# Kernel optimization log

Hardware: AMD Instinct MI355X
Metric: run time of the kernel (lower is better)

Reference implementation:

```python
import jax, jax.numpy as jnp
import numpy as np

N = 50000
E = 800000
IN_DIM = 128
LABEL_DIM = 32
D_MODEL = 128
REL_DIM = 32
NUM_LABELS = 1000
REL_BUCKETS = 1024
N_LAYERS = 2
EPS = 1e-5


def setup_inputs() -> dict:
    key = jax.random.key(0)
    ks = jax.random.split(key, 16)
    s = 0.02
    return {
        "x": jax.random.normal(ks[0], (N, IN_DIM), jnp.float32),
        "label": jax.random.randint(ks[1], (N,), 0, NUM_LABELS),
        "edge_index": jax.random.randint(ks[2], (2, E), 0, N),
        "edge_rel": jax.random.randint(ks[3], (E,), 0, REL_BUCKETS),
        "label_emb": jax.random.normal(ks[4], (NUM_LABELS, LABEL_DIM), jnp.float32) * s,
        "in_proj_w": jax.random.normal(ks[5], (IN_DIM + LABEL_DIM, D_MODEL), jnp.float32) * s,
        "in_proj_b": jnp.zeros((D_MODEL,), jnp.float32),
        "rel_emb": jax.random.normal(ks[6], (N_LAYERS, REL_BUCKETS, REL_DIM), jnp.float32) * s,
        "lin_neigh_w": jax.random.normal(ks[7], (N_LAYERS, D_MODEL, D_MODEL), jnp.float32) * s,
        "lin_self_w": jax.random.normal(ks[8], (N_LAYERS, D_MODEL, D_MODEL), jnp.float32) * s,
        "lin_self_b": jnp.zeros((N_LAYERS, D_MODEL), jnp.float32),
        "lin_rel_w": jax.random.normal(ks[9], (N_LAYERS, REL_DIM, D_MODEL), jnp.float32) * s,
        "ln_g": jnp.ones((N_LAYERS, D_MODEL), jnp.float32),
        "ln_b": jnp.zeros((N_LAYERS, D_MODEL), jnp.float32),
    }


def _layernorm(x, g, b):
    mu = jnp.mean(x, axis=-1, keepdims=True)
    var = jnp.mean(jnp.square(x - mu), axis=-1, keepdims=True)
    return (x - mu) * jax.lax.rsqrt(var + EPS) * g + b


def reference(x, label, edge_index, edge_rel, label_emb, in_proj_w, in_proj_b,
              rel_emb, lin_neigh_w, lin_self_w, lin_self_b, lin_rel_w, ln_g, ln_b):
    n = x.shape[0]
    src, dst = edge_index[0], edge_index[1]
    # input projection
    h = jnp.concatenate([x, label_emb[label]], axis=-1) @ in_proj_w + in_proj_b
    h = jax.nn.relu(h)
    # in-degree for mean aggregation (PyG 'mean' gives 0 for isolated nodes)
    deg = jax.ops.segment_sum(jnp.ones((src.shape[0],), h.dtype), dst, num_segments=n)
    inv_deg = jnp.where(deg > 0, 1.0 / jnp.maximum(deg, 1.0), 0.0)[:, None]
    for l in range(N_LAYERS):
        rel = rel_emb[l][edge_rel]                                   # [E, rel_dim]
        msg = h[src] @ lin_neigh_w[l] + rel @ lin_rel_w[l]           # [E, d]
        agg = jax.ops.segment_sum(msg, dst, num_segments=n) * inv_deg
        out = h @ lin_self_w[l] + lin_self_b[l] + agg
        h = _layernorm(jax.nn.relu(out), ln_g[l], ln_b[l])
    return h
```

## Files before the change

### kernel.cpp

```cpp
#include <hip/hip_runtime.h>
#include <hip/hip_bf16.h>

#define N_NODES 50000
#define N_EDGES 800000
#define D 128
#define LABEL_DIM 32
#define REL_DIM 32
#define REL_BUCKETS 1024
#define NUM_LABELS 1000
#define LN_EPS 1e-5f

#define NB 196
#define CAP 6144
#define EPB 1024

#define PB_IN 80
#define PB_LEMB 125
#define PB_CAT 144
#define PREP_UNITS (PB_IN + PB_LEMB + 2 * PB_CAT)

typedef short bf16x8 __attribute__((ext_vector_type(8)));
typedef float f32x4 __attribute__((ext_vector_type(4)));

__device__ inline unsigned short f2bf(float f) {
    __hip_bfloat16 h = __float2bfloat16(f);
    return *reinterpret_cast<unsigned short*>(&h);
}
__device__ inline float bf2f(unsigned short u) {
    return __uint_as_float((unsigned)u << 16);
}

__global__ __launch_bounds__(256) void prep_all_kernel(
    const float* __restrict__ in_proj_w, const float* __restrict__ label_emb,
    const float* __restrict__ lin_neigh_w, const float* __restrict__ lin_self_w,
    const float* __restrict__ lin_rel_w,
    unsigned short* __restrict__ Btx, unsigned short* __restrict__ leb,
    unsigned short* __restrict__ Btc0, unsigned short* __restrict__ Btc1,
    int* __restrict__ gcur) {
    int bb = blockIdx.x;
    const int t = threadIdx.x;
    if (bb == PREP_UNITS) {
        if (t < NB) gcur[t] = 0;
        return;
    }
    if (bb < PB_IN) {
        int idx = bb * 256 + t;
        int n = idx / 160, k = idx % 160;
        Btx[idx] = f2bf(in_proj_w[k * 128 + n]);
        return;
    }
    bb -= PB_IN;
    if (bb < PB_LEMB) {
        int i = bb * 256 + t;
        if (i < NUM_LABELS * LABEL_DIM) leb[i] = f2bf(label_emb[i]);
        return;
    }
    bb -= PB_LEMB;
    {
        int l = bb >= PB_CAT;
        if (l) bb -= PB_CAT;
        int idx = bb * 256 + t;
        int n = idx / 288, k = idx % 288;
        const float* Ws = lin_self_w + (size_t)l * 128 * 128;
        const float* Wn = lin_neigh_w + (size_t)l * 128 * 128;
        const float* Wr = lin_rel_w + (size_t)l * REL_DIM * 128;
        float v = (k < 128) ? Ws[(size_t)k * 128 + n]
                : (k < 256) ? Wn[(size_t)(k - 128) * 128 + n]
                            : Wr[(size_t)(k - 256) * 128 + n];
        (l ? Btc1 : Btc0)[idx] = f2bf(v);
    }
}

__global__ __launch_bounds__(256) void bin_scatter_kernel(const int* __restrict__ src,
                                                          const int* __restrict__ dst,
                                                          const int* __restrict__ rel,
                                                          int* __restrict__ gcur,
                                                          unsigned* __restrict__ staged_pk,
                                                          unsigned char* __restrict__ staged_dl) {
    __shared__ int hist[NB];
    __shared__ int lcur[NB];
    const int t = threadIdx.x;
    for (int i = t; i < NB; i += 256) hist[i] = 0;
    __syncthreads();
    const int e0 = blockIdx.x * EPB;
    unsigned char bb[4], dl[4];
#pragma unroll
    for (int i = 0; i < 4; ++i) {
        int e = e0 + i * 256 + t;
        if (e < N_EDGES) {
            int d = dst[e];
            bb[i] = (unsigned char)(d >> 8);
            dl[i] = (unsigned char)(d & 255);
            atomicAdd(&hist[d >> 8], 1);
        }
    }
    __syncthreads();
    for (int b = t; b < NB; b += 256) {
        int hc = hist[b];
        lcur[b] = hc ? (b * CAP + atomicAdd(&gcur[b], hc)) : 0;
    }
    __syncthreads();
#pragma unroll
    for (int i = 0; i < 4; ++i) {
        int e = e0 + i * 256 + t;
        if (e < N_EDGES) {
            int pos = atomicAdd(&lcur[bb[i]], 1);
            staged_pk[pos] = (unsigned)src[e] | ((unsigned)rel[e] << 16);
            staged_dl[pos] = dl[i];
        }
    }
}

__global__ __launch_bounds__(256) void place_in_kernel(
    const int* __restrict__ gcur,
    const unsigned* __restrict__ staged_pk, const unsigned char* __restrict__ staged_dl,
    int* __restrict__ off, int* __restrict__ deg, unsigned* __restrict__ csr_pk,
    const float* __restrict__ X, const unsigned short* __restrict__ Btx,
    const unsigned short* __restrict__ leb, const int* __restrict__ label,
    const float* __restrict__ bias, unsigned short* __restrict__ hb) {
    __shared__ __align__(16) char smem[128 * 160 * 2];
    const int t = threadIdx.x;
    const int bid = blockIdx.x;

    if (bid < NB) {
        int* ph = (int*)smem;
        int* pbuf = ph + 256;
        int* pcur = pbuf + 256;
        const int beg = bid * CAP;
        const int end = beg + gcur[bid];
        ph[t] = 0;
        __syncthreads();
        for (int i = beg + t; i < end; i += 256) atomicAdd(&ph[staged_dl[i]], 1);
        __syncthreads();
        int v = ph[t];
        pbuf[t] = v;
        __syncthreads();
        for (int o = 1; o < 256; o <<= 1) {
            int tv = (t >= o) ? pbuf[t - o] : 0;
            __syncthreads();
            pbuf[t] += tv;
            __syncthreads();
        }
        int node_off = beg + pbuf[t] - v;
        int node = bid * 256 + t;
        if (node < N_NODES) {
            off[node] = node_off;
            deg[node] = v;
        }
        pcur[t] = node_off;
        __syncthreads();
        for (int i = beg + t; i < end; i += 256) {
            int pos = atomicAdd(&pcur[staged_dl[i]], 1);
            csr_pk[pos] = staged_pk[i];
        }
        return;
    }

    unsigned short* sB = (unsigned short*)smem;
    const int mb = bid - NB;
#pragma unroll
    for (int i = 0; i < 10; ++i) {
        int c = t + i * 256;
        int col = c / 20, kch = c % 20;
        int dstc = col * 20 + (kch < 16 ? (kch ^ (col & 7)) : kch);
        *(bf16x8*)&sB[dstc * 8] = *(const bf16x8*)&Btx[c * 8];
    }
    __syncthreads();

    const int wave = t >> 6, lane = t & 63;
    const int m16 = lane & 15, q = lane >> 4;
    const int r0 = mb * 64 + wave * 16;
    const int arow = r0 + m16;
    const bool avalid = arow < N_NODES;
    const float* xp = X + (size_t)(avalid ? arow : 0) * 128 + q * 8;

    f32x4 acc[8];
#pragma unroll
    for (int ct = 0; ct < 8; ++ct) acc[ct] = (f32x4){0.f, 0.f, 0.f, 0.f};

#pragma unroll
    for (int ki = 0; ki < 4; ++ki) {
        bf16x8 af;
        if (avalid) {
            float4 v0 = *(const float4*)(xp + ki * 32);
            float4 v1 = *(const float4*)(xp + ki * 32 + 4);
            af[0] = (short)f2bf(v0.x); af[1] = (short)f2bf(v0.y);
            af[2] = (short)f2bf(v0.z); af[3] = (short)f2bf(v0.w);
            af[4] = (short)f2bf(v1.x); af[5] = (short)f2bf(v1.y);
            af[6] = (short)f2bf(v1.z); af[7] = (short)f2bf(v1.w);
        } else {
            af = (bf16x8){0, 0, 0, 0, 0, 0, 0, 0};
        }
        int kch = ki * 4 + q;
#pragma unroll
        for (int ct = 0; ct < 8; ++ct) {
            int col = ct * 16 + m16;
            int chunk = col * 20 + (kch ^ (m16 & 7));
            bf16x8 bf = *(const bf16x8*)&sB[chunk * 8];
            acc[ct] = __builtin_amdgcn_mfma_f32_16x16x32_bf16(af, bf, acc[ct], 0, 0, 0);
        }
    }
    {
        int lb = avalid ? label[arow] : 0;
        bf16x8 af = *(const bf16x8*)(leb + (size_t)lb * LABEL_DIM + q * 8);
        if (!avalid) af = (bf16x8){0, 0, 0, 0, 0, 0, 0, 0};
        int kch = 16 + q;
#pragma unroll
        for (int ct = 0; ct < 8; ++ct) {
            int col = ct * 16 + m16;
            int chunk = col * 20 + kch;
            bf16x8 bf = *(const bf16x8*)&sB[chunk * 8];
            acc[ct] = __builtin_amdgcn_mfma_f32_16x16x32_bf16(af, bf, acc[ct], 0, 0, 0);
        }
    }

#pragma unroll
    for (int ct = 0; ct < 8; ++ct) {
        int colg = ct * 16 + m16;
        float bs = bias[colg];
#pragma unroll
        for (int r = 0; r < 4; ++r) {
            int row = r0 + q * 4 + r;
            if (row < N_NODES) {
                float v = fmaxf(acc[ct][r] + bs, 0.f);
                hb[(size_t)row * 128 + colg] = f2bf(v);
            }
        }
    }
}

__global__ __launch_bounds__(256) void agg_raw_kernel(const unsigned short* __restrict__ hb,
                                                      const float* __restrict__ rel_emb_l,
                                                      const int* __restrict__ off,
                                                      const int* __restrict__ deg,
                                                      const unsigned* __restrict__ csr_pk,
                                                      unsigned short* __restrict__ Sm,
                                                      unsigned short* __restrict__ Rm) {
    const int wave = threadIdx.x >> 6;
    const int lane = threadIdx.x & 63;
    const int node = blockIdx.x * 4 + wave;
    if (node >= N_NODES) return;
    const int q = lane >> 4, l16 = lane & 15;
    const int beg = off[node];
    const int dcnt = deg[node];
    const int end = beg + dcnt;
    const int co = l16 * 8;

    float acc[8];
    float ra0 = 0.f, ra1 = 0.f;
#pragma unroll
    for (int j = 0; j < 8; ++j) acc[j] = 0.f;

    for (int e = beg; e < end; e += 8) {
        int i0 = e + q, i1 = e + 4 + q;
        float m0 = 1.f, m1 = 1.f;
        if (i0 >= end) { i0 = beg; m0 = 0.f; }
        if (i1 >= end) { i1 = beg; m1 = 0.f; }
        unsigned pk0 = csr_pk[i0];
        unsigned pk1 = csr_pk[i1];
        bf16x8 hv0 = *(const bf16x8*)(hb + ((size_t)(pk0 & 0xffffu) << 7) + co);
        bf16x8 hv1 = *(const bf16x8*)(hb + ((size_t)(pk1 & 0xffffu) << 7) + co);
        float2 rv0 = *(const float2*)(rel_emb_l + ((size_t)(pk0 >> 16) << 5) + l16 * 2);
        float2 rv1 = *(const float2*)(rel_emb_l + ((size_t)(pk1 >> 16) << 5) + l16 * 2);
#pragma unroll
        for (int j = 0; j < 8; ++j) acc[j] = fmaf(m0, bf2f((unsigned short)hv0[j]), acc[j]);
#pragma unroll
        for (int j = 0; j < 8; ++j) acc[j] = fmaf(m1, bf2f((unsigned short)hv1[j]), acc[j]);
        ra0 = fmaf(m0, rv0.x, ra0);
        ra1 = fmaf(m0, rv0.y, ra1);
        ra0 = fmaf(m1, rv1.x, ra0);
        ra1 = fmaf(m1, rv1.y, ra1);
    }
#pragma unroll
    for (int j = 0; j < 8; ++j) {
        acc[j] += __shfl_xor(acc[j], 16);
        acc[j] += __shfl_xor(acc[j], 32);
    }
    ra0 += __shfl_xor(ra0, 16); ra0 += __shfl_xor(ra0, 32);
    ra1 += __shfl_xor(ra1, 16); ra1 += __shfl_xor(ra1, 32);

    float inv = (dcnt > 0) ? 1.f / (float)dcnt : 0.f;
    if (q == 0) {
        bf16x8 ob;
#pragma unroll
        for (int j = 0; j < 8; ++j) ob[j] = (short)f2bf(acc[j] * inv);
        *(bf16x8*)(Sm + ((size_t)node << 7) + co) = ob;
        unsigned pk = (unsigned)f2bf(ra0 * inv) | ((unsigned)f2bf(ra1 * inv) << 16);
        ((unsigned*)(Rm + ((size_t)node << 5)))[l16] = pk;
    }
}

template <bool LAST>
__global__ __launch_bounds__(256) void gemm_ln_kernel(const unsigned short* __restrict__ Btc,
                                                      unsigned short* __restrict__ hb,
                                                      const unsigned short* __restrict__ Sm,
                                                      const unsigned short* __restrict__ Rm,
                                                      const float* __restrict__ bias,
                                                      const float* __restrict__ g,
                                                      const float* __restrict__ b,
                                                      float* __restrict__ hout) {
    __shared__ unsigned short sB[128 * 36 * 8];
    const int t = threadIdx.x;
#pragma unroll
    for (int i = 0; i < 18; ++i) {
        int c = t + i * 256;
        int col = c / 36, kch = c % 36;
        int swz = (kch < 32) ? (kch ^ (col & 7)) : (32 + ((kch - 32) ^ (col & 3)));
        *(bf16x8*)&sB[(col * 36 + swz) * 8] = *(const bf16x8*)&Btc[c * 8];
    }
    __syncthreads();

    const int wave = t >> 6, lane = t & 63;
    const int m16 = lane & 15, q = lane >> 4;
    const int r0 = blockIdx.x * 64 + wave * 16;
    const int arow = r0 + m16;
    const bool avalid = arow < N_NODES;
    const int sr = avalid ? arow : 0;
    const unsigned short* hp = hb + (size_t)sr * 128 + q * 8;
    const unsigned short* sp = Sm + (size_t)sr * 128 + q * 8;
    const unsigned short* rp = Rm + (size_t)sr * 32 + q * 8;

    f32x4 acc[8];
#pragma unroll
    for (int ct = 0; ct < 8; ++ct) acc[ct] = (f32x4){0.f, 0.f, 0.f, 0.f};
    const bf16x8 zf = (bf16x8){0, 0, 0, 0, 0, 0, 0, 0};

#pragma unroll
    for (int ki = 0; ki < 4; ++ki) {
        bf16x8 af = *(const bf16x8*)(hp + ki * 32);
        if (!avalid) af = zf;
        int kch = ki * 4 + q;
#pragma unroll
        for (int ct = 0; ct < 8; ++ct) {
            int col = ct * 16 + m16;
            bf16x8 bf = *(const bf16x8*)&sB[(col * 36 + (kch ^ (m16 & 7))) * 8];
            acc[ct] = __builtin_amdgcn_mfma_f32_16x16x32_bf16(af, bf, acc[ct], 0, 0, 0);
        }
    }
#pragma unroll
    for (int ki = 0; ki < 4; ++ki) {
        bf16x8 af = *(const bf16x8*)(sp + ki * 32);
        if (!avalid) af = zf;
        int kch = 16 + ki * 4 + q;
#pragma unroll
        for (int ct = 0; ct < 8; ++ct) {
            int col = ct * 16 + m16;
            bf16x8 bf = *(const bf16x8*)&sB[(col * 36 + (kch ^ (m16 & 7))) * 8];
            acc[ct] = __builtin_amdgcn_mfma_f32_16x16x32_bf16(af, bf, acc[ct], 0, 0, 0);
        }
    }
    {
        bf16x8 af = *(const bf16x8*)rp;
        if (!avalid) af = zf;
#pragma unroll
        for (int ct = 0; ct < 8; ++ct) {
            int col = ct * 16 + m16;
            bf16x8 bf = *(const bf16x8*)&sB[(col * 36 + 32 + (q ^ (m16 & 3))) * 8];
            acc[ct] = __builtin_amdgcn_mfma_f32_16x16x32_bf16(af, bf, acc[ct], 0, 0, 0);
        }
    }

    float bs[8], gs[8], bbs[8];
#pragma unroll
    for (int ct = 0; ct < 8; ++ct) {
        int cg2 = ct * 16 + m16;
        bs[ct] = bias[cg2];
        gs[ct] = g[cg2];
        bbs[ct] = b[cg2];
    }
#pragma unroll
    for (int r = 0; r < 4; ++r) {
        int row = r0 + q * 4 + r;
        float v[8];
        float s = 0.f;
#pragma unroll
        for (int ct = 0; ct < 8; ++ct) {
            float val = fmaxf(acc[ct][r] + bs[ct], 0.f);
            v[ct] = val;
            s += val;
        }
#pragma unroll
        for (int o = 8; o > 0; o >>= 1) s += __shfl_xor(s, o);
        float mu = s * (1.f / 128.f);
        float qs = 0.f;
#pragma unroll
        for (int ct = 0; ct < 8; ++ct) {
            float dd = v[ct] - mu;
            v[ct] = dd;
            qs += dd * dd;
        }
#pragma unroll
        for (int o = 8; o > 0; o >>= 1) qs += __shfl_xor(qs, o);
        float rstd = rsqrtf(qs * (1.f / 128.f) + LN_EPS);
        if (row < N_NODES) {
#pragma unroll
            for (int ct = 0; ct < 8; ++ct) {
                int colg = ct * 16 + m16;
                float o2 = v[ct] * rstd * gs[ct] + bbs[ct];
                if constexpr (LAST) {
                    hout[(size_t)row * 128 + colg] = o2;
                } else {
                    hb[(size_t)row * 128 + colg] = f2bf(o2);
                }
            }
        }
    }
}


extern "C" void kernel_launch(void* const* d_in, const int* in_sizes, int n_in,
                              void* d_out, int out_size, void* d_ws, size_t ws_size,
                              hipStream_t stream) {
    const float* x          = (const float*)d_in[0];
    const int*   label      = (const int*)d_in[1];
    const int*   edge_index = (const int*)d_in[2];
    const int*   edge_rel   = (const int*)d_in[3];
    const float* label_emb  = (const float*)d_in[4];
    const float* in_proj_w  = (const float*)d_in[5];
    const float* in_proj_b  = (const float*)d_in[6];
    const float* rel_emb    = (const float*)d_in[7];
    const float* lin_neigh_w = (const float*)d_in[8];
    const float* lin_self_w  = (const float*)d_in[9];
    const float* lin_self_b  = (const float*)d_in[10];
    const float* lin_rel_w   = (const float*)d_in[11];
    const float* ln_g        = (const float*)d_in[12];
    const float* ln_b        = (const float*)d_in[13];
    float* h = (float*)d_out;

    char* p = (char*)d_ws;
    auto alloc = [&](size_t bytes) {
        char* r = p;
        p += (bytes + 255) & ~(size_t)255;
        return r;
    };
    int* gcur        = (int*)alloc((size_t)NB * 4);
    int* off         = (int*)alloc((size_t)N_NODES * 4);
    int* deg         = (int*)alloc((size_t)N_NODES * 4);
    unsigned* csr_pk = (unsigned*)alloc((size_t)NB * CAP * 4);
    unsigned* staged_pk = (unsigned*)alloc((size_t)NB * CAP * 4);
    unsigned char* staged_dl = (unsigned char*)alloc((size_t)NB * CAP);
    unsigned short* hb  = (unsigned short*)alloc((size_t)N_NODES * 128 * 2);
    unsigned short* Sm  = (unsigned short*)alloc((size_t)N_NODES * 128 * 2);
    unsigned short* Rm  = (unsigned short*)alloc((size_t)N_NODES * 32 * 2);
    unsigned short* Btx = (unsigned short*)alloc((size_t)128 * 160 * 2);
    unsigned short* leb = (unsigned short*)alloc((size_t)NUM_LABELS * LABEL_DIM * 2);
    unsigned short* Btc0 = (unsigned short*)alloc((size_t)128 * 288 * 2);
    unsigned short* Btc1 = (unsigned short*)alloc((size_t)128 * 288 * 2);

    const int* src = edge_index;
    const int* dst = edge_index + N_EDGES;

    prep_all_kernel<<<PREP_UNITS + 1, 256, 0, stream>>>(
        in_proj_w, label_emb, lin_neigh_w, lin_self_w, lin_rel_w,
        Btx, leb, Btc0, Btc1, gcur);

    bin_scatter_kernel<<<(N_EDGES + EPB - 1) / EPB, 256, 0, stream>>>(
        src, dst, edge_rel, gcur, staged_pk, staged_dl);

    place_in_kernel<<<NB + (N_NODES + 63) / 64, 256, 0, stream>>>(
        gcur, staged_pk, staged_dl, off, deg, csr_pk,
        x, Btx, leb, label, in_proj_b, hb);

    const int gemm_grid = (N_NODES + 63) / 64;
    const int agg_grid = (N_NODES + 3) / 4;

    agg_raw_kernel<<<agg_grid, 256, 0, stream>>>(
        hb, rel_emb, off, deg, csr_pk, Sm, Rm);
    gemm_ln_kernel<false><<<gemm_grid, 256, 0, stream>>>(
        Btc0, hb, Sm, Rm, lin_self_b, ln_g, ln_b, nullptr);
    agg_raw_kernel<<<agg_grid, 256, 0, stream>>>(
        hb, rel_emb + (size_t)REL_BUCKETS * REL_DIM, off, deg, csr_pk, Sm, Rm);
    gemm_ln_kernel<true><<<gemm_grid, 256, 0, stream>>>(
        Btc1, hb, Sm, Rm, lin_self_b + 128, ln_g + 128, ln_b + 128, h);
}
```

Measured before the change: 251.6 us.

## Gather neighbor features in FP8 and fuse prep with edge scatter

Node features are additionally written as FP8 (e4m3) copies from the input-projection and layer GEMM epilogues, via a shared-memory bounce. The aggregation kernel now gathers these 8-bit rows, and a bf16 copy of the relation embedding, instead of bf16/fp32 data. This halves the per-edge gather traffic. The weight-prep kernel is merged into the edge-binning kernel, and the counter reset moves to a memset. The trade-off is reduced precision in the neighbor sums and an extra byte-per-element write plus a shared-memory round trip in the epilogues.

```diff
diff --git a/kernel.cpp b/kernel.cpp
--- a/kernel.cpp
+++ b/kernel.cpp
@@ -13,14 +13,21 @@
 #define NB 196
 #define CAP 6144
 #define EPB 1024
+#define NE_BLOCKS 782
 
 #define PB_IN 80
 #define PB_LEMB 125
 #define PB_CAT 144
-#define PREP_UNITS (PB_IN + PB_LEMB + 2 * PB_CAT)
+#define PB_REL 32
+#define PREP_UNITS (PB_IN + PB_LEMB + 2 * PB_CAT + 2 * PB_REL)
+
+#define BSTR 144
 
 typedef short bf16x8 __attribute__((ext_vector_type(8)));
 typedef float f32x4 __attribute__((ext_vector_type(4)));
+typedef float f32x2 __attribute__((ext_vector_type(2)));
+typedef unsigned int u32x2 __attribute__((ext_vector_type(2)));
+typedef unsigned int u32x4 __attribute__((ext_vector_type(4)));
 
 __device__ inline unsigned short f2bf(float f) {
     __hip_bfloat16 h = __float2bfloat16(f);
@@ -30,59 +37,76 @@
     return __uint_as_float((unsigned)u << 16);
 }
 
-__global__ __launch_bounds__(256) void prep_all_kernel(
+__device__ inline void pack8_fp8(const bf16x8 bv, unsigned& lo, unsigned& hi) {
+    float f0 = bf2f((unsigned short)bv[0]), f1 = bf2f((unsigned short)bv[1]);
+    float f2 = bf2f((unsigned short)bv[2]), f3 = bf2f((unsigned short)bv[3]);
+    float f4 = bf2f((unsigned short)bv[4]), f5 = bf2f((unsigned short)bv[5]);
+    float f6 = bf2f((unsigned short)bv[6]), f7 = bf2f((unsigned short)bv[7]);
+    lo = __builtin_amdgcn_cvt_pk_fp8_f32(f0, f1, 0u, false);
+    lo = __builtin_amdgcn_cvt_pk_fp8_f32(f2, f3, lo, true);
+    hi = __builtin_amdgcn_cvt_pk_fp8_f32(f4, f5, 0u, false);
+    hi = __builtin_amdgcn_cvt_pk_fp8_f32(f6, f7, hi, true);
+}
+
+__global__ __launch_bounds__(256) void scatter_prep_kernel(
+    const int* __restrict__ src, const int* __restrict__ dst, const int* __restrict__ rel,
+    int* __restrict__ gcur, unsigned* __restrict__ staged_pk, unsigned char* __restrict__ staged_dl,
     const float* __restrict__ in_proj_w, const float* __restrict__ label_emb,
     const float* __restrict__ lin_neigh_w, const float* __restrict__ lin_self_w,
-    const float* __restrict__ lin_rel_w,
+    const float* __restrict__ lin_rel_w, const float* __restrict__ rel_emb,
     unsigned short* __restrict__ Btx, unsigned short* __restrict__ leb,
     unsigned short* __restrict__ Btc0, unsigned short* __restrict__ Btc1,
-    int* __restrict__ gcur) {
-    int bb = blockIdx.x;
-    const int t = threadIdx.x;
-    if (bb == PREP_UNITS) {
-        if (t < NB) gcur[t] = 0;
-        return;
-    }
-    if (bb < PB_IN) {
-        int idx = bb * 256 + t;
-        int n = idx / 160, k = idx % 160;
-        Btx[idx] = f2bf(in_proj_w[k * 128 + n]);
-        return;
-    }
-    bb -= PB_IN;
-    if (bb < PB_LEMB) {
-        int i = bb * 256 + t;
-        if (i < NUM_LABELS * LABEL_DIM) leb[i] = f2bf(label_emb[i]);
-        return;
-    }
-    bb -= PB_LEMB;
-    {
-        int l = bb >= PB_CAT;
-        if (l) bb -= PB_CAT;
-        int idx = bb * 256 + t;
-        int n = idx / 288, k = idx % 288;
-        const float* Ws = lin_self_w + (size_t)l * 128 * 128;
-        const float* Wn = lin_neigh_w + (size_t)l * 128 * 128;
-        const float* Wr = lin_rel_w + (size_t)l * REL_DIM * 128;
-        float v = (k < 128) ? Ws[(size_t)k * 128 + n]
-                : (k < 256) ? Wn[(size_t)(k - 128) * 128 + n]
-                            : Wr[(size_t)(k - 256) * 128 + n];
-        (l ? Btc1 : Btc0)[idx] = f2bf(v);
-    }
-}
-
-__global__ __launch_bounds__(256) void bin_scatter_kernel(const int* __restrict__ src,
-                                                          const int* __restrict__ dst,
-                                                          const int* __restrict__ rel,
-                                                          int* __restrict__ gcur,
-                                                          unsigned* __restrict__ staged_pk,
-                                                          unsigned char* __restrict__ staged_dl) {
+    unsigned short* __restrict__ relb0, unsigned short* __restrict__ relb1) {
     __shared__ int hist[NB];
     __shared__ int lcur[NB];
     const int t = threadIdx.x;
+    const int bid = blockIdx.x;
+
+    if (bid >= NE_BLOCKS) {
+        int u = bid - NE_BLOCKS;
+        if (u < PB_IN) {
+            int idx = u * 256 + t;
+            int n = idx / 160, k = idx % 160;
+            Btx[idx] = f2bf(in_proj_w[k * 128 + n]);
+            return;
+        }
+        u -= PB_IN;
+        if (u < PB_LEMB) {
+            int i = u * 256 + t;
+            if (i < NUM_LABELS * LABEL_DIM) leb[i] = f2bf(label_emb[i]);
+            return;
+        }
+        u -= PB_LEMB;
+        if (u < 2 * PB_CAT) {
+            int l = u >= PB_CAT;
+            int cb = l ? u - PB_CAT : u;
+            int idx = cb * 256 + t;
+            int n = idx / 288, k = idx % 288;
+            const float* Ws = lin_self_w + (size_t)l * 128 * 128;
+            const float* Wn = lin_neigh_w + (size_t)l * 128 * 128;
+            const float* Wr = lin_rel_w + (size_t)l * REL_DIM * 128;
+            float v = (k < 128) ? Ws[(size_t)k * 128 + n]
+                    : (k < 256) ? Wn[(size_t)(k - 128) * 128 + n]
+                                : Wr[(size_t)(k - 256) * 128 + n];
+            (l ? Btc1 : Btc0)[idx] = f2bf(v);
+            return;
+        }
+        u -= 2 * PB_CAT;
+        {
+            int l = u >= PB_REL;
+            int rb = l ? u - PB_REL : u;
+            int idx = rb * 1024 + t * 4;
+            float4 v = *(const float4*)(rel_emb + (size_t)l * REL_BUCKETS * REL_DIM + idx);
+            unsigned short* out = (l ? relb1 : relb0) + idx;
+            out[0] = f2bf(v.x); out[1] = f2bf(v.y);
+            out[2] = f2bf(v.z); out[3] = f2bf(v.w);
+            return;
+        }
+    }
+
     for (int i = t; i < NB; i += 256) hist[i] = 0;
     __syncthreads();
-    const int e0 = blockIdx.x * EPB;
+    const int e0 = bid * EPB;
     unsigned char bb[4], dl[4];
 #pragma unroll
     for (int i = 0; i < 4; ++i) {
@@ -117,7 +141,8 @@
     int* __restrict__ off, int* __restrict__ deg, unsigned* __restrict__ csr_pk,
     const float* __restrict__ X, const unsigned short* __restrict__ Btx,
     const unsigned short* __restrict__ leb, const int* __restrict__ label,
-    const float* __restrict__ bias, unsigned short* __restrict__ hb) {
+    const float* __restrict__ bias, unsigned short* __restrict__ hb,
+    unsigned char* __restrict__ hb8) {
     __shared__ __align__(16) char smem[128 * 160 * 2];
     const int t = threadIdx.x;
     const int bid = blockIdx.x;
@@ -214,6 +239,7 @@
         }
     }
 
+    unsigned short hbv[8][4];
 #pragma unroll
     for (int ct = 0; ct < 8; ++ct) {
         int colg = ct * 16 + m16;
@@ -221,16 +247,42 @@
 #pragma unroll
         for (int r = 0; r < 4; ++r) {
             int row = r0 + q * 4 + r;
-            if (row < N_NODES) {
-                float v = fmaxf(acc[ct][r] + bs, 0.f);
-                hb[(size_t)row * 128 + colg] = f2bf(v);
+            float v = fmaxf(acc[ct][r] + bs, 0.f);
+            hbv[ct][r] = f2bf(v);
+            if (row < N_NODES) hb[(size_t)row * 128 + colg] = hbv[ct][r];
+        }
+    }
+
+    __syncthreads();
+    unsigned short* bounce = sB;
+#pragma unroll
+    for (int ct = 0; ct < 8; ++ct) {
+        int colg = ct * 16 + m16;
+#pragma unroll
+        for (int r = 0; r < 4; ++r)
+            bounce[(wave * 16 + q * 4 + r) * BSTR + colg] = hbv[ct][r];
+    }
+    __syncthreads();
+    {
+        int rl = t >> 2;
+        int grow = mb * 64 + rl;
+        if (grow < N_NODES) {
+            const unsigned short* bp = bounce + rl * BSTR + (t & 3) * 32;
+            unsigned o[8];
+#pragma unroll
+            for (int k = 0; k < 4; ++k) {
+                bf16x8 bv = *(const bf16x8*)(bp + k * 8);
+                pack8_fp8(bv, o[2 * k], o[2 * k + 1]);
             }
-        }
-    }
-}
-
-__global__ __launch_bounds__(256) void agg_raw_kernel(const unsigned short* __restrict__ hb,
-                                                      const float* __restrict__ rel_emb_l,
+            u32x4* dp = (u32x4*)(hb8 + (size_t)grow * 128 + (t & 3) * 32);
+            dp[0] = (u32x4){o[0], o[1], o[2], o[3]};
+            dp[1] = (u32x4){o[4], o[5], o[6], o[7]};
+        }
+    }
+}
+
+__global__ __launch_bounds__(256) void agg_raw_kernel(const unsigned char* __restrict__ hb8,
+                                                      const unsigned short* __restrict__ relb,
                                                       const int* __restrict__ off,
                                                       const int* __restrict__ deg,
                                                       const unsigned* __restrict__ csr_pk,
@@ -258,18 +310,34 @@
         if (i1 >= end) { i1 = beg; m1 = 0.f; }
         unsigned pk0 = csr_pk[i0];
         unsigned pk1 = csr_pk[i1];
-        bf16x8 hv0 = *(const bf16x8*)(hb + ((size_t)(pk0 & 0xffffu) << 7) + co);
-        bf16x8 hv1 = *(const bf16x8*)(hb + ((size_t)(pk1 & 0xffffu) << 7) + co);
-        float2 rv0 = *(const float2*)(rel_emb_l + ((size_t)(pk0 >> 16) << 5) + l16 * 2);
-        float2 rv1 = *(const float2*)(rel_emb_l + ((size_t)(pk1 >> 16) << 5) + l16 * 2);
-#pragma unroll
-        for (int j = 0; j < 8; ++j) acc[j] = fmaf(m0, bf2f((unsigned short)hv0[j]), acc[j]);
-#pragma unroll
-        for (int j = 0; j < 8; ++j) acc[j] = fmaf(m1, bf2f((unsigned short)hv1[j]), acc[j]);
-        ra0 = fmaf(m0, rv0.x, ra0);
-        ra1 = fmaf(m0, rv0.y, ra1);
-        ra0 = fmaf(m1, rv1.x, ra0);
-        ra1 = fmaf(m1, rv1.y, ra1);
+        u32x2 hv0 = *(const u32x2*)(hb8 + ((size_t)(pk0 & 0xffffu) << 7) + co);
+        u32x2 hv1 = *(const u32x2*)(hb8 + ((size_t)(pk1 & 0xffffu) << 7) + co);
+        unsigned rw0 = *(const unsigned*)(relb + ((size_t)(pk0 >> 16) << 5) + l16 * 2);
+        unsigned rw1 = *(const unsigned*)(relb + ((size_t)(pk1 >> 16) << 5) + l16 * 2);
+        {
+            f32x2 d0 = __builtin_amdgcn_cvt_pk_f32_fp8(hv0[0], false);
+            f32x2 d1 = __builtin_amdgcn_cvt_pk_f32_fp8(hv0[0], true);
+            f32x2 d2 = __builtin_amdgcn_cvt_pk_f32_fp8(hv0[1], false);
+            f32x2 d3 = __builtin_amdgcn_cvt_pk_f32_fp8(hv0[1], true);
+            acc[0] = fmaf(m0, d0[0], acc[0]); acc[1] = fmaf(m0, d0[1], acc[1]);
+            acc[2] = fmaf(m0, d1[0], acc[2]); acc[3] = fmaf(m0, d1[1], acc[3]);
+            acc[4] = fmaf(m0, d2[0], acc[4]); acc[5] = fmaf(m0, d2[1], acc[5]);
+            acc[6] = fmaf(m0, d3[0], acc[6]); acc[7] = fmaf(m0, d3[1], acc[7]);
+        }
+        {
+            f32x2 d0 = __builtin_amdgcn_cvt_pk_f32_fp8(hv1[0], false);
+            f32x2 d1 = __builtin_amdgcn_cvt_pk_f32_fp8(hv1[0], true);
+            f32x2 d2 = __builtin_amdgcn_cvt_pk_f32_fp8(hv1[1], false);
+            f32x2 d3 = __builtin_amdgcn_cvt_pk_f32_fp8(hv1[1], true);
+            acc[0] = fmaf(m1, d0[0], acc[0]); acc[1] = fmaf(m1, d0[1], acc[1]);
+            acc[2] = fmaf(m1, d1[0], acc[2]); acc[3] = fmaf(m1, d1[1], acc[3]);
+            acc[4] = fmaf(m1, d2[0], acc[4]); acc[5] = fmaf(m1, d2[1], acc[5]);
+            acc[6] = fmaf(m1, d3[0], acc[6]); acc[7] = fmaf(m1, d3[1], acc[7]);
+        }
+        ra0 = fmaf(m0, bf2f((unsigned short)(rw0 & 0xffffu)), ra0);
+        ra1 = fmaf(m0, bf2f((unsigned short)(rw0 >> 16)), ra1);
+        ra0 = fmaf(m1, bf2f((unsigned short)(rw1 & 0xffffu)), ra0);
+        ra1 = fmaf(m1, bf2f((unsigned short)(rw1 >> 16)), ra1);
     }
 #pragma unroll
     for (int j = 0; j < 8; ++j) {
@@ -293,6 +361,7 @@
 template <bool LAST>
 __global__ __launch_bounds__(256) void gemm_ln_kernel(const unsigned short* __restrict__ Btc,
                                                       unsigned short* __restrict__ hb,
+                                                      unsigned char* __restrict__ hb8,
                                                       const unsigned short* __restrict__ Sm,
                                                       const unsigned short* __restrict__ Rm,
                                                       const float* __restrict__ bias,
@@ -368,6 +437,7 @@
         gs[ct] = g[cg2];
         bbs[ct] = b[cg2];
     }
+    unsigned short hbv[4][8];
 #pragma unroll
     for (int r = 0; r < 4; ++r) {
         int row = r0 + q * 4 + r;
@@ -392,17 +462,45 @@
 #pragma unroll
         for (int o = 8; o > 0; o >>= 1) qs += __shfl_xor(qs, o);
         float rstd = rsqrtf(qs * (1.f / 128.f) + LN_EPS);
-        if (row < N_NODES) {
-#pragma unroll
-            for (int ct = 0; ct < 8; ++ct) {
-                int colg = ct * 16 + m16;
-                float o2 = v[ct] * rstd * gs[ct] + bbs[ct];
+#pragma unroll
+        for (int ct = 0; ct < 8; ++ct) {
+            int colg = ct * 16 + m16;
+            float o2 = v[ct] * rstd * gs[ct] + bbs[ct];
+            hbv[r][ct] = f2bf(o2);
+            if (row < N_NODES) {
                 if constexpr (LAST) {
                     hout[(size_t)row * 128 + colg] = o2;
                 } else {
-                    hb[(size_t)row * 128 + colg] = f2bf(o2);
+                    hb[(size_t)row * 128 + colg] = hbv[r][ct];
                 }
             }
+        }
+    }
+
+    if constexpr (!LAST) {
+        __syncthreads();
+        unsigned short* bounce = sB;
+#pragma unroll
+        for (int r = 0; r < 4; ++r) {
+            int rl = wave * 16 + q * 4 + r;
+#pragma unroll
+            for (int ct = 0; ct < 8; ++ct)
+                bounce[rl * BSTR + ct * 16 + m16] = hbv[r][ct];
+        }
+        __syncthreads();
+        int rl = t >> 2;
+        int grow = blockIdx.x * 64 + rl;
+        if (grow < N_NODES) {
+            const unsigned short* bp = bounce + rl * BSTR + (t & 3) * 32;
+            unsigned o[8];
+#pragma unroll
+            for (int k = 0; k < 4; ++k) {
+                bf16x8 bv = *(const bf16x8*)(bp + k * 8);
+                pack8_fp8(bv, o[2 * k], o[2 * k + 1]);
+            }
+            u32x4* dp = (u32x4*)(hb8 + (size_t)grow * 128 + (t & 3) * 32);
+            dp[0] = (u32x4){o[0], o[1], o[2], o[3]};
+            dp[1] = (u32x4){o[4], o[5], o[6], o[7]};
         }
     }
 }
@@ -440,36 +538,39 @@
     unsigned* staged_pk = (unsigned*)alloc((size_t)NB * CAP * 4);
     unsigned char* staged_dl = (unsigned char*)alloc((size_t)NB * CAP);
     unsigned short* hb  = (unsigned short*)alloc((size_t)N_NODES * 128 * 2);
+    unsigned char*  hb8 = (unsigned char*)alloc((size_t)N_NODES * 128);
     unsigned short* Sm  = (unsigned short*)alloc((size_t)N_NODES * 128 * 2);
     unsigned short* Rm  = (unsigned short*)alloc((size_t)N_NODES * 32 * 2);
     unsigned short* Btx = (unsigned short*)alloc((size_t)128 * 160 * 2);
     unsigned short* leb = (unsigned short*)alloc((size_t)NUM_LABELS * LABEL_DIM * 2);
     unsigned short* Btc0 = (unsigned short*)alloc((size_t)128 * 288 * 2);
     unsigned short* Btc1 = (unsigned short*)alloc((size_t)128 * 288 * 2);
+    unsigned short* relb0 = (unsigned short*)alloc((size_t)REL_BUCKETS * REL_DIM * 2);
+    unsigned short* relb1 = (unsigned short*)alloc((size_t)REL_BUCKETS * REL_DIM * 2);
 
     const int* src = edge_index;
     const int* dst = edge_index + N_EDGES;
 
-    prep_all_kernel<<<PREP_UNITS + 1, 256, 0, stream>>>(
-        in_proj_w, label_emb, lin_neigh_w, lin_self_w, lin_rel_w,
-        Btx, leb, Btc0, Btc1, gcur);
-
-    bin_scatter_kernel<<<(N_EDGES + EPB - 1) / EPB, 256, 0, stream>>>(
-        src, dst, edge_rel, gcur, staged_pk, staged_dl);
-
-    place_in_kernel<<<NB + (N_NODES + 63) / 64, 256, 0, stream>>>(
+    hipMemsetAsync(gcur, 0, (size_t)NB * 4, stream);
+
+    scatter_prep_kernel<<<NE_BLOCKS + PREP_UNITS, 256, 0, stream>>>(
+        src, dst, edge_rel, gcur, staged_pk, staged_dl,
+        in_proj_w, label_emb, lin_neigh_w, lin_self_w, lin_rel_w, rel_emb,
+        Btx, leb, Btc0, Btc1, relb0, relb1);
+
+    place_in_kernel<<<NB + NE_BLOCKS, 256, 0, stream>>>(
         gcur, staged_pk, staged_dl, off, deg, csr_pk,
-        x, Btx, leb, label, in_proj_b, hb);
+        x, Btx, leb, label, in_proj_b, hb, hb8);
 
     const int gemm_grid = (N_NODES + 63) / 64;
     const int agg_grid = (N_NODES + 3) / 4;
 
     agg_raw_kernel<<<agg_grid, 256, 0, stream>>>(
-        hb, rel_emb, off, deg, csr_pk, Sm, Rm);
+        hb8, relb0, off, deg, csr_pk, Sm, Rm);
     gemm_ln_kernel<false><<<gemm_grid, 256, 0, stream>>>(
-        Btc0, hb, Sm, Rm, lin_self_b, ln_g, ln_b, nullptr);
+        Btc0, hb, hb8, Sm, Rm, lin_self_b, ln_g, ln_b, nullptr);
     agg_raw_kernel<<<agg_grid, 256, 0, stream>>>(
-        hb, rel_emb + (size_t)REL_BUCKETS * REL_DIM, off, deg, csr_pk, Sm, Rm);
+        hb8, relb1, off, deg, csr_pk, Sm, Rm);
     gemm_ln_kernel<true><<<gemm_grid, 256, 0, stream>>>(
-        Btc1, hb, Sm, Rm, lin_self_b + 128, ln_g + 128, ln_b + 128, h);
-}
+        Btc1, hb, hb8, Sm, Rm, lin_self_b + 128, ln_g + 128, ln_b + 128, h);
+}
```

New measurement: 246.1 us. -2.2%, faster.
